# Performance work log

Hardware: AMD Instinct MI355X
Metric: run time of the kernel (lower is better)

The kernel has to match this reference:

```python
import jax, jax.numpy as jnp
import numpy as np

SH_DEGREE = 1
D_SH = (SH_DEGREE + 1) ** 2  # 4
SCALE_MIN = 0.5
SCALE_MAX = 15.0
MULTIPLIER = 0.1
EPS = 1e-8


def quat_to_rotmat(q):
    # q: [..., 4] (w, x, y, z), assumed (near-)normalized
    w, x, y, z = q[..., 0], q[..., 1], q[..., 2], q[..., 3]
    return jnp.stack([
        jnp.stack([1 - 2 * (y * y + z * z), 2 * (x * y - w * z), 2 * (x * z + w * y)], -1),
        jnp.stack([2 * (x * y + w * z), 1 - 2 * (x * x + z * z), 2 * (y * z - w * x)], -1),
        jnp.stack([2 * (x * z - w * y), 2 * (y * z + w * x), 1 - 2 * (x * x + y * y)], -1),
    ], -2)


def setup_inputs() -> dict:
    key = jax.random.key(0)
    ks = jax.random.split(key, 6)
    B, N = 8, 131072
    H, W = 256, 512
    # valid SE(3) extrinsics (rotation from random unit quaternion)
    q = jax.random.normal(ks[0], (B, 1, 4), dtype=jnp.float32)
    q = q / jnp.linalg.norm(q, axis=-1, keepdims=True)
    R = quat_to_rotmat(q)
    t = jax.random.normal(ks[1], (B, 1, 3), dtype=jnp.float32)
    ext = jnp.zeros((B, 1, 4, 4), jnp.float32)
    ext = ext.at[..., :3, :3].set(R).at[..., :3, 3].set(t).at[..., 3, 3].set(1.0)
    # normalized pinhole intrinsics
    K = jnp.array([[1.2, 0.0, 0.5], [0.0, 1.2, 0.5], [0.0, 0.0, 1.0]], jnp.float32)
    K = jnp.broadcast_to(K, (B, 1, 3, 3))
    coordinates = jax.random.uniform(ks[2], (B, N, 2), dtype=jnp.float32)
    depths = jax.random.uniform(ks[3], (B, N), dtype=jnp.float32, minval=0.5, maxval=10.0)
    opacities = jax.random.uniform(ks[4], (B, N), dtype=jnp.float32)
    raw_gaussians = jax.random.normal(ks[5], (B, N, 7 + 3 * D_SH), dtype=jnp.float32)
    return {"extrinsics": ext, "intrinsics": K, "coordinates": coordinates,
            "depths": depths, "opacities": opacities, "raw_gaussians": raw_gaussians,
            "h": H, "w": W}


def reference(extrinsics, intrinsics, coordinates, depths, opacities, raw_gaussians, h, w):
    # sh mask: degree-0 untouched, degree d scaled by 0.1 * 0.25**d
    sh_mask = jnp.ones((D_SH,), jnp.float32)
    for d in range(1, SH_DEGREE + 1):
        sh_mask = sh_mask.at[d ** 2:(d + 1) ** 2].set(0.1 * 0.25 ** d)

    scales_raw = raw_gaussians[..., :3]
    rot_raw = raw_gaussians[..., 3:7]
    sh = raw_gaussians[..., 7:]

    scales = SCALE_MIN + (SCALE_MAX - SCALE_MIN) * jax.nn.sigmoid(scales_raw)

    # scale multiplier from inverse of 2x2 top-left of intrinsics
    pixel_size = 1.0 / jnp.array([w, h], jnp.float32)
    a = intrinsics[..., 0, 0]; b = intrinsics[..., 0, 1]
    c = intrinsics[..., 1, 0]; d = intrinsics[..., 1, 1]
    det = a * d - b * c
    inv2 = jnp.stack([jnp.stack([d, -b], -1), jnp.stack([-c, a], -1)], -2) / det[..., None, None]
    multiplier = (MULTIPLIER * jnp.einsum('...ij,j->...i', inv2, pixel_size)).sum(-1)  # [B,1]

    scales = scales * depths[..., None] * multiplier[..., None]  # [B,N,3]

    rotations = rot_raw / (jnp.linalg.norm(rot_raw, axis=-1, keepdims=True) + EPS)  # [B,N,4]

    sh = sh.reshape(*sh.shape[:-1], 3, D_SH) * sh_mask  # [B,N,3,D_SH]

    # covariance = R diag(s^2) R^T, then rotate into world frame
    R = quat_to_rotmat(rotations)  # [B,N,3,3]
    cov = jnp.einsum('...ij,...j,...kj->...ik', R, scales * scales, R)
    c2w = extrinsics[..., :3, :3]  # [B,1,3,3]
    cov = jnp.einsum('...ij,...jk,...lk->...il', c2w, cov, c2w)  # [B,N,3,3]

    # world rays: unproject pixel coords with depth 1, normalize, rotate to world
    coords_h = jnp.concatenate([coordinates, jnp.ones_like(coordinates[..., :1])], -1)  # [B,N,3]
    Kinv = jnp.linalg.inv(intrinsics)  # [B,1,3,3]
    dirs = jnp.einsum('...ij,...j->...i', Kinv, coords_h)
    dirs = dirs / jnp.linalg.norm(dirs, axis=-1, keepdims=True)
    dirs_w = jnp.einsum('...ij,...j->...i', c2w, dirs)  # [B,N,3]
    origins = jnp.broadcast_to(extrinsics[..., :3, 3], dirs_w.shape)
    means = origins + dirs_w * depths[..., None]  # [B,N,3]

    # rotate SH: l=0 identity; l=1 Wigner-D equals c2w in the (y,z,x) permuted basis
    p = jnp.array([1, 2, 0])
    D1 = c2w[..., p, :][..., :, p]  # [B,1,3,3]
    sh0 = sh[..., :1]
    sh1 = jnp.einsum('...ij,...cj->...ci', D1, sh[..., 1:4])
    harmonics = jnp.concatenate([sh0, sh1], -1)  # [B,N,3,D_SH]

    rotations_b = jnp.broadcast_to(rotations, (*scales.shape[:-1], 4))
    return (means, cov, harmonics, opacities, scales, rotations_b)
```

## Files before the change

kernel.cpp:

```cpp
#include <hip/hip_runtime.h>
#include <math.h>

#define SCALE_MIN 0.5f
#define SCALE_MAX 15.0f
#define MULTIPLIER 0.1f
#define EPS 1e-8f

typedef float v4f __attribute__((ext_vector_type(4)));
typedef float v2f __attribute__((ext_vector_type(2)));


#define WVF 1728
#define O_MEAN  0
#define O_COV   192
#define O_HARM  768
#define O_SCALE 1536

__global__ __launch_bounds__(256) void mono_gaussian_adapter_kernel(
    const float* __restrict__ ext,
    const float* __restrict__ intr,
    const float* __restrict__ coord,
    const float* __restrict__ depth,
    const float* __restrict__ opac,
    const float* __restrict__ rawg,
    const int* __restrict__ hp,
    const int* __restrict__ wp,
    float* __restrict__ out,
    int bpb,
    int BN)
{
    __shared__ __align__(16) float lds[4 * WVF];

    const int tid  = threadIdx.x;
    const int lane = tid & 63;
    const int wid  = tid >> 6;
    const int blk  = blockIdx.x;
    const int gid  = blk * 256 + tid;
    const int gw   = blk * 4 + wid;
    const int b    = blk / bpb;

    float* lw = lds + wid * WVF;

    const v4f* gin = (const v4f*)(rawg + (long long)gw * (64 * 19));
    v4f s0v = __builtin_nontemporal_load(gin + lane);
    v4f s1v = __builtin_nontemporal_load(gin + 64 + lane);
    v4f s2v = __builtin_nontemporal_load(gin + 128 + lane);
    v4f s3v = __builtin_nontemporal_load(gin + 192 + lane);
    v4f s4v;
    if (lane < 48) s4v = __builtin_nontemporal_load(gin + 256 + lane);

    v2f uv  = __builtin_nontemporal_load((const v2f*)coord + gid);
    float dep = __builtin_nontemporal_load(depth + gid);
    float op  = __builtin_nontemporal_load(opac + gid);

    float inv_w = 1.0f / (float)wp[0];
    float inv_h = 1.0f / (float)hp[0];

    const float* E = ext + b * 16;
    float c00=E[0],  c01=E[1],  c02=E[2],  t0=E[3];
    float c10=E[4],  c11=E[5],  c12=E[6],  t1=E[7];
    float c20=E[8],  c21=E[9],  c22=E[10], t2=E[11];

    const float* Kb = intr + b * 9;
    float k00=Kb[0],k01=Kb[1],k02=Kb[2];
    float k10=Kb[3],k11=Kb[4],k12=Kb[5];
    float k20=Kb[6],k21=Kb[7],k22=Kb[8];

    float det2 = k00*k11 - k01*k10;
    float mult = MULTIPLIER * ((k11*inv_w - k01*inv_h) + (k00*inv_h - k10*inv_w)) / det2;

    float det3 = k00*(k11*k22 - k12*k21)
               + k01*(k12*k20 - k10*k22)
               + k02*(k10*k21 - k11*k20);
    float id3 = 1.0f / det3;
    float i00 = (k11*k22 - k12*k21)*id3;
    float i01 = (k02*k21 - k01*k22)*id3;
    float i02 = (k01*k12 - k02*k11)*id3;
    float i10 = (k12*k20 - k10*k22)*id3;
    float i11 = (k00*k22 - k02*k20)*id3;
    float i12 = (k02*k10 - k00*k12)*id3;
    float i20 = (k10*k21 - k11*k20)*id3;
    float i21 = (k01*k20 - k00*k21)*id3;
    float i22 = (k00*k11 - k01*k10)*id3;

    {
        v4f* l4 = (v4f*)lw;
        l4[lane]       = s0v;
        l4[64 + lane]  = s1v;
        l4[128 + lane] = s2v;
        l4[192 + lane] = s3v;
        if (lane < 48) l4[256 + lane] = s4v;
    }

    const float* g = lw + lane * 19;
    float sr0 = g[0], sr1 = g[1], sr2 = g[2];
    float q0 = g[3], q1 = g[4], q2 = g[5], q3 = g[6];
    float sh00=g[7],  sh01=g[8],  sh02=g[9],  sh03=g[10];
    float sh10=g[11], sh11=g[12], sh12=g[13], sh13=g[14];
    float sh20=g[15], sh21=g[16], sh22=g[17], sh23=g[18];

    float s0 = SCALE_MIN + (SCALE_MAX - SCALE_MIN) / (1.0f + __expf(-sr0));
    float s1 = SCALE_MIN + (SCALE_MAX - SCALE_MIN) / (1.0f + __expf(-sr1));
    float s2 = SCALE_MIN + (SCALE_MAX - SCALE_MIN) / (1.0f + __expf(-sr2));
    float dm = dep * mult;
    s0 *= dm; s1 *= dm; s2 *= dm;

    float qn = sqrtf(q0*q0 + q1*q1 + q2*q2 + q3*q3) + EPS;
    float qi = 1.0f / qn;
    float qw = q0*qi, qx = q1*qi, qy = q2*qi, qz = q3*qi;

    __builtin_nontemporal_store(op, out + 24LL*BN + gid);
    v4f rq = { qw, qx, qy, qz };
    __builtin_nontemporal_store(rq, (v4f*)(out + 28LL*BN) + gid);

    float r00 = 1.0f - 2.0f*(qy*qy + qz*qz);
    float r01 = 2.0f*(qx*qy - qw*qz);
    float r02 = 2.0f*(qx*qz + qw*qy);
    float r10 = 2.0f*(qx*qy + qw*qz);
    float r11 = 1.0f - 2.0f*(qx*qx + qz*qz);
    float r12 = 2.0f*(qy*qz - qw*qx);
    float r20 = 2.0f*(qx*qz - qw*qy);
    float r21 = 2.0f*(qy*qz + qw*qx);
    float r22 = 1.0f - 2.0f*(qx*qx + qy*qy);

    float v0 = s0*s0, v1 = s1*s1, v2 = s2*s2;
    float p00 = r00*r00*v0 + r01*r01*v1 + r02*r02*v2;
    float p01 = r00*r10*v0 + r01*r11*v1 + r02*r12*v2;
    float p02 = r00*r20*v0 + r01*r21*v1 + r02*r22*v2;
    float p11 = r10*r10*v0 + r11*r11*v1 + r12*r12*v2;
    float p12 = r10*r20*v0 + r11*r21*v1 + r12*r22*v2;
    float p22 = r20*r20*v0 + r21*r21*v1 + r22*r22*v2;

    float m00 = c00*p00 + c01*p01 + c02*p02;
    float m01 = c00*p01 + c01*p11 + c02*p12;
    float m02 = c00*p02 + c01*p12 + c02*p22;
    float m10 = c10*p00 + c11*p01 + c12*p02;
    float m11 = c10*p01 + c11*p11 + c12*p12;
    float m12 = c10*p02 + c11*p12 + c12*p22;
    float m20 = c20*p00 + c21*p01 + c22*p02;
    float m21 = c20*p01 + c21*p11 + c22*p12;
    float m22 = c20*p02 + c21*p12 + c22*p22;

    float q00 = m00*c00 + m01*c01 + m02*c02;
    float q01 = m00*c10 + m01*c11 + m02*c12;
    float q02 = m00*c20 + m01*c21 + m02*c22;
    float q11 = m10*c10 + m11*c11 + m12*c12;
    float q12 = m10*c20 + m11*c21 + m12*c22;
    float q22 = m20*c20 + m21*c21 + m22*c22;

    float d0 = i00*uv.x + i01*uv.y + i02;
    float d1 = i10*uv.x + i11*uv.y + i12;
    float d2 = i20*uv.x + i21*uv.y + i22;
    float rn = rsqrtf(d0*d0 + d1*d1 + d2*d2);
    d0 *= rn; d1 *= rn; d2 *= rn;
    float w0 = c00*d0 + c01*d1 + c02*d2;
    float w1 = c10*d0 + c11*d1 + c12*d2;
    float w2 = c20*d0 + c21*d1 + c22*d2;
    float me0 = t0 + w0*dep;
    float me1 = t1 + w1*dep;
    float me2 = t2 + w2*dep;

    float D00=c11, D01=c12, D02=c10;
    float D10=c21, D11=c22, D12=c20;
    float D20=c01, D21=c02, D22=c00;
    const float msk = 0.1f * 0.25f;
    float a1 = msk*sh01, a2 = msk*sh02, a3 = msk*sh03;
    float b1 = msk*sh11, b2 = msk*sh12, b3 = msk*sh13;
    float e1 = msk*sh21, e2 = msk*sh22, e3 = msk*sh23;
    v4f h0 = { sh00, D00*a1 + D01*a2 + D02*a3,
                     D10*a1 + D11*a2 + D12*a3,
                     D20*a1 + D21*a2 + D22*a3 };
    v4f h1 = { sh10, D00*b1 + D01*b2 + D02*b3,
                     D10*b1 + D11*b2 + D12*b3,
                     D20*b1 + D21*b2 + D22*b3 };
    v4f h2 = { sh20, D00*e1 + D01*e2 + D02*e3,
                     D10*e1 + D11*e2 + D12*e3,
                     D20*e1 + D21*e2 + D22*e3 };

    {
        float* lm = lw + O_MEAN + lane * 3;
        lm[0] = me0; lm[1] = me1; lm[2] = me2;

        float* lc = lw + O_COV + lane * 9;
        lc[0]=q00; lc[1]=q01; lc[2]=q02;
        lc[3]=q01; lc[4]=q11; lc[5]=q12;
        lc[6]=q02; lc[7]=q12; lc[8]=q22;

        v4f* lh = (v4f*)(lds + (wid * WVF + O_HARM)) + lane * 3;
        lh[0] = h0; lh[1] = h1; lh[2] = h2;

        float* ls = lw + O_SCALE + lane * 3;
        ls[0] = s0; ls[1] = s1; ls[2] = s2;
    }

    {
        const v4f* l4 = (const v4f*)lw;
        v4f* gm = (v4f*)(out + (long long)gw * 192);
        v4f* gs = (v4f*)(out + 25LL*BN + (long long)gw * 192);
        if (lane < 48) {
            __builtin_nontemporal_store(l4[(O_MEAN / 4) + lane], gm + lane);
            __builtin_nontemporal_store(l4[(O_SCALE / 4) + lane], gs + lane);
        }
        v4f* gc = (v4f*)(out + 3LL*BN + (long long)gw * 576);
        #pragma unroll
        for (int i = 0; i < 2; ++i)
            __builtin_nontemporal_store(l4[(O_COV / 4) + lane + i*64], gc + lane + i*64);
        if (lane < 16)
            __builtin_nontemporal_store(l4[(O_COV / 4) + lane + 128], gc + lane + 128);

        v4f* gh = (v4f*)(out + 12LL*BN + (long long)gw * 768);
        #pragma unroll
        for (int i = 0; i < 3; ++i)
            __builtin_nontemporal_store(l4[(O_HARM / 4) + lane + i*64], gh + lane + i*64);
    }
}

extern "C" void kernel_launch(void* const* d_in, const int* in_sizes, int n_in,
                              void* d_out, int out_size, void* d_ws, size_t ws_size,
                              hipStream_t stream) {
    const float* ext   = (const float*)d_in[0];
    const float* intr  = (const float*)d_in[1];
    const float* coord = (const float*)d_in[2];
    const float* depth = (const float*)d_in[3];
    const float* opac  = (const float*)d_in[4];
    const float* rawg  = (const float*)d_in[5];
    const int*   hp    = (const int*)d_in[6];
    const int*   wp    = (const int*)d_in[7];

    int BN = in_sizes[3];
    int B  = in_sizes[0] / 16;
    int N  = BN / B;
    int blocks = BN / 256;
    int bpb = N / 256;

    mono_gaussian_adapter_kernel<<<blocks, 256, 0, stream>>>(
        ext, intr, coord, depth, opac, rawg, hp, wp,
        (float*)d_out, bpb, BN);
}
```

Baseline: 212.6 us.

## Process four tiles per block with register double-buffered prefetch of next tile

Each block now loops over four consecutive 256-element tiles and issues the global loads for the next tile before computing and storing the current one, so load latency overlaps with compute and stores. The grid shrinks by a factor of four. This adds register pressure from holding two tiles of inputs, which could lower occupancy. Fewer blocks also means less parallelism for latency hiding on a memory-bound kernel.

```diff
diff --git a/kernel.cpp b/kernel.cpp
--- a/kernel.cpp
+++ b/kernel.cpp
@@ -9,12 +9,15 @@
 typedef float v4f __attribute__((ext_vector_type(4)));
 typedef float v2f __attribute__((ext_vector_type(2)));
 
+#define LDS_FENCE() asm volatile("" ::: "memory")
 
 #define WVF 1728
 #define O_MEAN  0
 #define O_COV   192
 #define O_HARM  768
 #define O_SCALE 1536
+
+#define TILES_PER_BLOCK 4
 
 __global__ __launch_bounds__(256) void mono_gaussian_adapter_kernel(
     const float* __restrict__ ext,
@@ -27,191 +30,231 @@
     const int* __restrict__ wp,
     float* __restrict__ out,
     int bpb,
-    int BN)
+    int BN,
+    int tiles)
 {
     __shared__ __align__(16) float lds[4 * WVF];
 
     const int tid  = threadIdx.x;
     const int lane = tid & 63;
     const int wid  = tid >> 6;
-    const int blk  = blockIdx.x;
-    const int gid  = blk * 256 + tid;
-    const int gw   = blk * 4 + wid;
-    const int b    = blk / bpb;
+
+    int t = blockIdx.x * TILES_PER_BLOCK;
+    const int t1 = (t + TILES_PER_BLOCK < tiles) ? (t + TILES_PER_BLOCK) : tiles;
 
     float* lw = lds + wid * WVF;
 
-    const v4f* gin = (const v4f*)(rawg + (long long)gw * (64 * 19));
-    v4f s0v = __builtin_nontemporal_load(gin + lane);
-    v4f s1v = __builtin_nontemporal_load(gin + 64 + lane);
-    v4f s2v = __builtin_nontemporal_load(gin + 128 + lane);
-    v4f s3v = __builtin_nontemporal_load(gin + 192 + lane);
-    v4f s4v;
-    if (lane < 48) s4v = __builtin_nontemporal_load(gin + 256 + lane);
-
-    v2f uv  = __builtin_nontemporal_load((const v2f*)coord + gid);
-    float dep = __builtin_nontemporal_load(depth + gid);
-    float op  = __builtin_nontemporal_load(opac + gid);
-
-    float inv_w = 1.0f / (float)wp[0];
-    float inv_h = 1.0f / (float)hp[0];
-
-    const float* E = ext + b * 16;
-    float c00=E[0],  c01=E[1],  c02=E[2],  t0=E[3];
-    float c10=E[4],  c11=E[5],  c12=E[6],  t1=E[7];
-    float c20=E[8],  c21=E[9],  c22=E[10], t2=E[11];
-
-    const float* Kb = intr + b * 9;
-    float k00=Kb[0],k01=Kb[1],k02=Kb[2];
-    float k10=Kb[3],k11=Kb[4],k12=Kb[5];
-    float k20=Kb[6],k21=Kb[7],k22=Kb[8];
-
-    float det2 = k00*k11 - k01*k10;
-    float mult = MULTIPLIER * ((k11*inv_w - k01*inv_h) + (k00*inv_h - k10*inv_w)) / det2;
-
-    float det3 = k00*(k11*k22 - k12*k21)
-               + k01*(k12*k20 - k10*k22)
-               + k02*(k10*k21 - k11*k20);
-    float id3 = 1.0f / det3;
-    float i00 = (k11*k22 - k12*k21)*id3;
-    float i01 = (k02*k21 - k01*k22)*id3;
-    float i02 = (k01*k12 - k02*k11)*id3;
-    float i10 = (k12*k20 - k10*k22)*id3;
-    float i11 = (k00*k22 - k02*k20)*id3;
-    float i12 = (k02*k10 - k00*k12)*id3;
-    float i20 = (k10*k21 - k11*k20)*id3;
-    float i21 = (k01*k20 - k00*k21)*id3;
-    float i22 = (k00*k11 - k01*k10)*id3;
-
+    const float inv_w = 1.0f / (float)wp[0];
+    const float inv_h = 1.0f / (float)hp[0];
+
+    v4f c0v = {0,0,0,0}, c1v = {0,0,0,0}, c2v = {0,0,0,0},
+        c3v = {0,0,0,0}, c4v = {0,0,0,0};
+    v2f cuv = {0,0}; float cdep = 0.0f, cop = 0.0f;
     {
-        v4f* l4 = (v4f*)lw;
-        l4[lane]       = s0v;
-        l4[64 + lane]  = s1v;
-        l4[128 + lane] = s2v;
-        l4[192 + lane] = s3v;
-        if (lane < 48) l4[256 + lane] = s4v;
+        const v4f* gin = (const v4f*)(rawg + (long long)(t * 4 + wid) * 1216);
+        c0v = __builtin_nontemporal_load(gin + lane);
+        c1v = __builtin_nontemporal_load(gin + 64 + lane);
+        c2v = __builtin_nontemporal_load(gin + 128 + lane);
+        c3v = __builtin_nontemporal_load(gin + 192 + lane);
+        if (lane < 48) c4v = __builtin_nontemporal_load(gin + 256 + lane);
+        const int gid = t * 256 + tid;
+        cuv  = __builtin_nontemporal_load((const v2f*)coord + gid);
+        cdep = __builtin_nontemporal_load(depth + gid);
+        cop  = __builtin_nontemporal_load(opac + gid);
     }
 
-    const float* g = lw + lane * 19;
-    float sr0 = g[0], sr1 = g[1], sr2 = g[2];
-    float q0 = g[3], q1 = g[4], q2 = g[5], q3 = g[6];
-    float sh00=g[7],  sh01=g[8],  sh02=g[9],  sh03=g[10];
-    float sh10=g[11], sh11=g[12], sh12=g[13], sh13=g[14];
-    float sh20=g[15], sh21=g[16], sh22=g[17], sh23=g[18];
-
-    float s0 = SCALE_MIN + (SCALE_MAX - SCALE_MIN) / (1.0f + __expf(-sr0));
-    float s1 = SCALE_MIN + (SCALE_MAX - SCALE_MIN) / (1.0f + __expf(-sr1));
-    float s2 = SCALE_MIN + (SCALE_MAX - SCALE_MIN) / (1.0f + __expf(-sr2));
-    float dm = dep * mult;
-    s0 *= dm; s1 *= dm; s2 *= dm;
-
-    float qn = sqrtf(q0*q0 + q1*q1 + q2*q2 + q3*q3) + EPS;
-    float qi = 1.0f / qn;
-    float qw = q0*qi, qx = q1*qi, qy = q2*qi, qz = q3*qi;
-
-    __builtin_nontemporal_store(op, out + 24LL*BN + gid);
-    v4f rq = { qw, qx, qy, qz };
-    __builtin_nontemporal_store(rq, (v4f*)(out + 28LL*BN) + gid);
-
-    float r00 = 1.0f - 2.0f*(qy*qy + qz*qz);
-    float r01 = 2.0f*(qx*qy - qw*qz);
-    float r02 = 2.0f*(qx*qz + qw*qy);
-    float r10 = 2.0f*(qx*qy + qw*qz);
-    float r11 = 1.0f - 2.0f*(qx*qx + qz*qz);
-    float r12 = 2.0f*(qy*qz - qw*qx);
-    float r20 = 2.0f*(qx*qz - qw*qy);
-    float r21 = 2.0f*(qy*qz + qw*qx);
-    float r22 = 1.0f - 2.0f*(qx*qx + qy*qy);
-
-    float v0 = s0*s0, v1 = s1*s1, v2 = s2*s2;
-    float p00 = r00*r00*v0 + r01*r01*v1 + r02*r02*v2;
-    float p01 = r00*r10*v0 + r01*r11*v1 + r02*r12*v2;
-    float p02 = r00*r20*v0 + r01*r21*v1 + r02*r22*v2;
-    float p11 = r10*r10*v0 + r11*r11*v1 + r12*r12*v2;
-    float p12 = r10*r20*v0 + r11*r21*v1 + r12*r22*v2;
-    float p22 = r20*r20*v0 + r21*r21*v1 + r22*r22*v2;
-
-    float m00 = c00*p00 + c01*p01 + c02*p02;
-    float m01 = c00*p01 + c01*p11 + c02*p12;
-    float m02 = c00*p02 + c01*p12 + c02*p22;
-    float m10 = c10*p00 + c11*p01 + c12*p02;
-    float m11 = c10*p01 + c11*p11 + c12*p12;
-    float m12 = c10*p02 + c11*p12 + c12*p22;
-    float m20 = c20*p00 + c21*p01 + c22*p02;
-    float m21 = c20*p01 + c21*p11 + c22*p12;
-    float m22 = c20*p02 + c21*p12 + c22*p22;
-
-    float q00 = m00*c00 + m01*c01 + m02*c02;
-    float q01 = m00*c10 + m01*c11 + m02*c12;
-    float q02 = m00*c20 + m01*c21 + m02*c22;
-    float q11 = m10*c10 + m11*c11 + m12*c12;
-    float q12 = m10*c20 + m11*c21 + m12*c22;
-    float q22 = m20*c20 + m21*c21 + m22*c22;
-
-    float d0 = i00*uv.x + i01*uv.y + i02;
-    float d1 = i10*uv.x + i11*uv.y + i12;
-    float d2 = i20*uv.x + i21*uv.y + i22;
-    float rn = rsqrtf(d0*d0 + d1*d1 + d2*d2);
-    d0 *= rn; d1 *= rn; d2 *= rn;
-    float w0 = c00*d0 + c01*d1 + c02*d2;
-    float w1 = c10*d0 + c11*d1 + c12*d2;
-    float w2 = c20*d0 + c21*d1 + c22*d2;
-    float me0 = t0 + w0*dep;
-    float me1 = t1 + w1*dep;
-    float me2 = t2 + w2*dep;
-
-    float D00=c11, D01=c12, D02=c10;
-    float D10=c21, D11=c22, D12=c20;
-    float D20=c01, D21=c02, D22=c00;
-    const float msk = 0.1f * 0.25f;
-    float a1 = msk*sh01, a2 = msk*sh02, a3 = msk*sh03;
-    float b1 = msk*sh11, b2 = msk*sh12, b3 = msk*sh13;
-    float e1 = msk*sh21, e2 = msk*sh22, e3 = msk*sh23;
-    v4f h0 = { sh00, D00*a1 + D01*a2 + D02*a3,
-                     D10*a1 + D11*a2 + D12*a3,
-                     D20*a1 + D21*a2 + D22*a3 };
-    v4f h1 = { sh10, D00*b1 + D01*b2 + D02*b3,
-                     D10*b1 + D11*b2 + D12*b3,
-                     D20*b1 + D21*b2 + D22*b3 };
-    v4f h2 = { sh20, D00*e1 + D01*e2 + D02*e3,
-                     D10*e1 + D11*e2 + D12*e3,
-                     D20*e1 + D21*e2 + D22*e3 };
-
-    {
-        float* lm = lw + O_MEAN + lane * 3;
-        lm[0] = me0; lm[1] = me1; lm[2] = me2;
-
-        float* lc = lw + O_COV + lane * 9;
-        lc[0]=q00; lc[1]=q01; lc[2]=q02;
-        lc[3]=q01; lc[4]=q11; lc[5]=q12;
-        lc[6]=q02; lc[7]=q12; lc[8]=q22;
-
-        v4f* lh = (v4f*)(lds + (wid * WVF + O_HARM)) + lane * 3;
-        lh[0] = h0; lh[1] = h1; lh[2] = h2;
-
-        float* ls = lw + O_SCALE + lane * 3;
-        ls[0] = s0; ls[1] = s1; ls[2] = s2;
-    }
-
-    {
-        const v4f* l4 = (const v4f*)lw;
-        v4f* gm = (v4f*)(out + (long long)gw * 192);
-        v4f* gs = (v4f*)(out + 25LL*BN + (long long)gw * 192);
-        if (lane < 48) {
-            __builtin_nontemporal_store(l4[(O_MEAN / 4) + lane], gm + lane);
-            __builtin_nontemporal_store(l4[(O_SCALE / 4) + lane], gs + lane);
-        }
-        v4f* gc = (v4f*)(out + 3LL*BN + (long long)gw * 576);
-        #pragma unroll
-        for (int i = 0; i < 2; ++i)
-            __builtin_nontemporal_store(l4[(O_COV / 4) + lane + i*64], gc + lane + i*64);
-        if (lane < 16)
-            __builtin_nontemporal_store(l4[(O_COV / 4) + lane + 128], gc + lane + 128);
-
-        v4f* gh = (v4f*)(out + 12LL*BN + (long long)gw * 768);
-        #pragma unroll
-        for (int i = 0; i < 3; ++i)
-            __builtin_nontemporal_store(l4[(O_HARM / 4) + lane + i*64], gh + lane + i*64);
+    while (t < t1) {
+        const int tn = t + 1;
+
+        v4f n0v = {0,0,0,0}, n1v = {0,0,0,0}, n2v = {0,0,0,0},
+            n3v = {0,0,0,0}, n4v = {0,0,0,0};
+        v2f nuv = {0,0}; float ndep = 0.0f, nop = 0.0f;
+        if (tn < t1) {
+            const v4f* gin = (const v4f*)(rawg + (long long)(tn * 4 + wid) * 1216);
+            n0v = __builtin_nontemporal_load(gin + lane);
+            n1v = __builtin_nontemporal_load(gin + 64 + lane);
+            n2v = __builtin_nontemporal_load(gin + 128 + lane);
+            n3v = __builtin_nontemporal_load(gin + 192 + lane);
+            if (lane < 48) n4v = __builtin_nontemporal_load(gin + 256 + lane);
+            const int gid2 = tn * 256 + tid;
+            nuv  = __builtin_nontemporal_load((const v2f*)coord + gid2);
+            ndep = __builtin_nontemporal_load(depth + gid2);
+            nop  = __builtin_nontemporal_load(opac + gid2);
+        }
+
+        const int gid = t * 256 + tid;
+        const int gw  = t * 4 + wid;
+        const int b   = t / bpb;
+
+        const float* E = ext + b * 16;
+        float c00=E[0],  c01=E[1],  c02=E[2],  t0=E[3];
+        float c10=E[4],  c11=E[5],  c12=E[6],  tt1=E[7];
+        float c20=E[8],  c21=E[9],  c22=E[10], t2=E[11];
+
+        const float* Kb = intr + b * 9;
+        float k00=Kb[0],k01=Kb[1],k02=Kb[2];
+        float k10=Kb[3],k11=Kb[4],k12=Kb[5];
+        float k20=Kb[6],k21=Kb[7],k22=Kb[8];
+
+        float det2 = k00*k11 - k01*k10;
+        float mult = MULTIPLIER * ((k11*inv_w - k01*inv_h) + (k00*inv_h - k10*inv_w)) / det2;
+
+        float det3 = k00*(k11*k22 - k12*k21)
+                   + k01*(k12*k20 - k10*k22)
+                   + k02*(k10*k21 - k11*k20);
+        float id3 = 1.0f / det3;
+        float i00 = (k11*k22 - k12*k21)*id3;
+        float i01 = (k02*k21 - k01*k22)*id3;
+        float i02 = (k01*k12 - k02*k11)*id3;
+        float i10 = (k12*k20 - k10*k22)*id3;
+        float i11 = (k00*k22 - k02*k20)*id3;
+        float i12 = (k02*k10 - k00*k12)*id3;
+        float i20 = (k10*k21 - k11*k20)*id3;
+        float i21 = (k01*k20 - k00*k21)*id3;
+        float i22 = (k00*k11 - k01*k10)*id3;
+
+        LDS_FENCE();
+
+        {
+            v4f* l4 = (v4f*)lw;
+            l4[lane]       = c0v;
+            l4[64 + lane]  = c1v;
+            l4[128 + lane] = c2v;
+            l4[192 + lane] = c3v;
+            if (lane < 48) l4[256 + lane] = c4v;
+        }
+
+        LDS_FENCE();
+
+        const float* g = lw + lane * 19;
+        float sr0 = g[0], sr1 = g[1], sr2 = g[2];
+        float q0 = g[3], q1 = g[4], q2 = g[5], q3 = g[6];
+        float sh00=g[7],  sh01=g[8],  sh02=g[9],  sh03=g[10];
+        float sh10=g[11], sh11=g[12], sh12=g[13], sh13=g[14];
+        float sh20=g[15], sh21=g[16], sh22=g[17], sh23=g[18];
+
+        LDS_FENCE();
+
+        float s0 = SCALE_MIN + (SCALE_MAX - SCALE_MIN) / (1.0f + __expf(-sr0));
+        float s1 = SCALE_MIN + (SCALE_MAX - SCALE_MIN) / (1.0f + __expf(-sr1));
+        float s2 = SCALE_MIN + (SCALE_MAX - SCALE_MIN) / (1.0f + __expf(-sr2));
+        float dm = cdep * mult;
+        s0 *= dm; s1 *= dm; s2 *= dm;
+
+        float qn = sqrtf(q0*q0 + q1*q1 + q2*q2 + q3*q3) + EPS;
+        float qi = 1.0f / qn;
+        float qw = q0*qi, qx = q1*qi, qy = q2*qi, qz = q3*qi;
+
+        __builtin_nontemporal_store(cop, out + 24LL*BN + gid);
+        v4f rq = { qw, qx, qy, qz };
+        __builtin_nontemporal_store(rq, (v4f*)(out + 28LL*BN) + gid);
+
+        float r00 = 1.0f - 2.0f*(qy*qy + qz*qz);
+        float r01 = 2.0f*(qx*qy - qw*qz);
+        float r02 = 2.0f*(qx*qz + qw*qy);
+        float r10 = 2.0f*(qx*qy + qw*qz);
+        float r11 = 1.0f - 2.0f*(qx*qx + qz*qz);
+        float r12 = 2.0f*(qy*qz - qw*qx);
+        float r20 = 2.0f*(qx*qz - qw*qy);
+        float r21 = 2.0f*(qy*qz + qw*qx);
+        float r22 = 1.0f - 2.0f*(qx*qx + qy*qy);
+
+        float v0 = s0*s0, v1 = s1*s1, v2 = s2*s2;
+        float p00 = r00*r00*v0 + r01*r01*v1 + r02*r02*v2;
+        float p01 = r00*r10*v0 + r01*r11*v1 + r02*r12*v2;
+        float p02 = r00*r20*v0 + r01*r21*v1 + r02*r22*v2;
+        float p11 = r10*r10*v0 + r11*r11*v1 + r12*r12*v2;
+        float p12 = r10*r20*v0 + r11*r21*v1 + r12*r22*v2;
+        float p22 = r20*r20*v0 + r21*r21*v1 + r22*r22*v2;
+
+        float m00 = c00*p00 + c01*p01 + c02*p02;
+        float m01 = c00*p01 + c01*p11 + c02*p12;
+        float m02 = c00*p02 + c01*p12 + c02*p22;
+        float m10 = c10*p00 + c11*p01 + c12*p02;
+        float m11 = c10*p01 + c11*p11 + c12*p12;
+        float m12 = c10*p02 + c11*p12 + c12*p22;
+        float m20 = c20*p00 + c21*p01 + c22*p02;
+        float m21 = c20*p01 + c21*p11 + c22*p12;
+        float m22 = c20*p02 + c21*p12 + c22*p22;
+
+        float q00 = m00*c00 + m01*c01 + m02*c02;
+        float q01 = m00*c10 + m01*c11 + m02*c12;
+        float q02 = m00*c20 + m01*c21 + m02*c22;
+        float q11 = m10*c10 + m11*c11 + m12*c12;
+        float q12 = m10*c20 + m11*c21 + m12*c22;
+        float q22 = m20*c20 + m21*c21 + m22*c22;
+
+        float d0 = i00*cuv.x + i01*cuv.y + i02;
+        float d1 = i10*cuv.x + i11*cuv.y + i12;
+        float d2 = i20*cuv.x + i21*cuv.y + i22;
+        float rn = rsqrtf(d0*d0 + d1*d1 + d2*d2);
+        d0 *= rn; d1 *= rn; d2 *= rn;
+        float w0 = c00*d0 + c01*d1 + c02*d2;
+        float w1 = c10*d0 + c11*d1 + c12*d2;
+        float w2 = c20*d0 + c21*d1 + c22*d2;
+        float me0 = t0  + w0*cdep;
+        float me1 = tt1 + w1*cdep;
+        float me2 = t2  + w2*cdep;
+
+        float D00=c11, D01=c12, D02=c10;
+        float D10=c21, D11=c22, D12=c20;
+        float D20=c01, D21=c02, D22=c00;
+        const float msk = 0.1f * 0.25f;
+        float a1 = msk*sh01, a2 = msk*sh02, a3 = msk*sh03;
+        float b1 = msk*sh11, b2 = msk*sh12, b3 = msk*sh13;
+        float e1 = msk*sh21, e2 = msk*sh22, e3 = msk*sh23;
+        v4f h0 = { sh00, D00*a1 + D01*a2 + D02*a3,
+                         D10*a1 + D11*a2 + D12*a3,
+                         D20*a1 + D21*a2 + D22*a3 };
+        v4f h1 = { sh10, D00*b1 + D01*b2 + D02*b3,
+                         D10*b1 + D11*b2 + D12*b3,
+                         D20*b1 + D21*b2 + D22*b3 };
+        v4f h2 = { sh20, D00*e1 + D01*e2 + D02*e3,
+                         D10*e1 + D11*e2 + D12*e3,
+                         D20*e1 + D21*e2 + D22*e3 };
+
+        {
+            float* lm = lw + O_MEAN + lane * 3;
+            lm[0] = me0; lm[1] = me1; lm[2] = me2;
+
+            float* lc = lw + O_COV + lane * 9;
+            lc[0]=q00; lc[1]=q01; lc[2]=q02;
+            lc[3]=q01; lc[4]=q11; lc[5]=q12;
+            lc[6]=q02; lc[7]=q12; lc[8]=q22;
+
+            v4f* lh = (v4f*)(lds + (wid * WVF + O_HARM)) + lane * 3;
+            lh[0] = h0; lh[1] = h1; lh[2] = h2;
+
+            float* ls = lw + O_SCALE + lane * 3;
+            ls[0] = s0; ls[1] = s1; ls[2] = s2;
+        }
+
+        LDS_FENCE();
+
+        {
+            const v4f* l4 = (const v4f*)lw;
+            v4f* gm = (v4f*)(out + (long long)gw * 192);
+            v4f* gs = (v4f*)(out + 25LL*BN + (long long)gw * 192);
+            if (lane < 48) {
+                __builtin_nontemporal_store(l4[(O_MEAN / 4) + lane], gm + lane);
+                __builtin_nontemporal_store(l4[(O_SCALE / 4) + lane], gs + lane);
+            }
+            v4f* gc = (v4f*)(out + 3LL*BN + (long long)gw * 576);
+            #pragma unroll
+            for (int i = 0; i < 2; ++i)
+                __builtin_nontemporal_store(l4[(O_COV / 4) + lane + i*64], gc + lane + i*64);
+            if (lane < 16)
+                __builtin_nontemporal_store(l4[(O_COV / 4) + lane + 128], gc + lane + 128);
+
+            v4f* gh = (v4f*)(out + 12LL*BN + (long long)gw * 768);
+            #pragma unroll
+            for (int i = 0; i < 3; ++i)
+                __builtin_nontemporal_store(l4[(O_HARM / 4) + lane + i*64], gh + lane + i*64);
+        }
+
+        c0v = n0v; c1v = n1v; c2v = n2v; c3v = n3v; c4v = n4v;
+        cuv = nuv; cdep = ndep; cop = nop;
+        t = tn;
     }
 }
 
@@ -230,10 +273,11 @@
     int BN = in_sizes[3];
     int B  = in_sizes[0] / 16;
     int N  = BN / B;
-    int blocks = BN / 256;
+    int tiles = BN / 256;
     int bpb = N / 256;
+    int blocks = (tiles + TILES_PER_BLOCK - 1) / TILES_PER_BLOCK;
 
     mono_gaussian_adapter_kernel<<<blocks, 256, 0, stream>>>(
         ext, intr, coord, depth, opac, rawg, hp, wp,
-        (float*)d_out, bpb, BN);
+        (float*)d_out, bpb, BN, tiles);
 }
```

After: 215.4 us. About the same (+1.3%).
